# Kernel optimization log

Hardware: AMD Instinct MI355X
Metric: run time of the kernel (lower is better)

Reference implementation:

```python
import jax, jax.numpy as jnp
import numpy as np

N_NODES = 100_000
N_EDGES = 1_600_000
D_IN = 128
D_OUT = 128


def setup_inputs() -> dict:
    key = jax.random.key(0)
    ks = jax.random.split(key, 6)
    X = jax.random.normal(ks[0], (N_NODES, D_IN), dtype=jnp.float32)
    ref_a = jax.random.randint(ks[1], (N_EDGES,), 0, N_NODES, dtype=jnp.int64 if jax.config.jax_enable_x64 else jnp.int32)
    backref = jax.random.randint(ks[2], (N_EDGES,), 0, N_NODES, dtype=jnp.int64 if jax.config.jax_enable_x64 else jnp.int32)
    e_map = jax.random.randint(ks[3], (N_EDGES,), 0, N_NODES, dtype=jnp.int32)
    v_count = jnp.ones((1,), dtype=jnp.int32)
    # GlorotUniform init for the two projection matrices
    limit = np.sqrt(6.0 / (D_IN + D_OUT)).astype(np.float32)
    W = jax.random.uniform(ks[4], (D_IN, D_OUT), dtype=jnp.float32, minval=-limit, maxval=limit)
    W_prop = jax.random.uniform(ks[5], (D_IN, D_OUT), dtype=jnp.float32, minval=-limit, maxval=limit)
    b = jnp.zeros((D_OUT,), dtype=jnp.float32)
    return {"X": X, "ref_a": ref_a, "backref": backref, "e_map": e_map,
            "v_count": v_count, "W": W, "W_prop": W_prop, "b": b}


def reference(X, ref_a, backref, e_map, v_count, W, W_prop, b):
    # Dual linear projections
    XW = X @ W                 # [N, D_OUT]
    XW_prop = X @ W_prop       # [N, D_OUT]
    # wl1_convolution_compact: gather rows at edge sources, scatter-sum into targets
    msgs = XW_prop[ref_a]      # [E, D_OUT] irregular gather
    X_conv = jax.ops.segment_sum(msgs, backref, num_segments=X.shape[0])  # [N, D_OUT]
    # bias add + activation
    X_out = jax.nn.relu(XW + X_conv + b)
    return (X_out, ref_a, backref, e_map, v_count)
```

## Files before the change

kernel.cpp:

```cpp
#include <hip/hip_runtime.h>
#include <hip/hip_bf16.h>


#define SCAN_BE 1024

typedef __attribute__((ext_vector_type(8))) short bf16x8;
typedef __attribute__((ext_vector_type(4))) float f32x4;

__device__ __forceinline__ float bf2f(unsigned short u) {
    return __uint_as_float(((unsigned int)u) << 16);
}

__device__ __forceinline__ unsigned short f2bf(float f) {
    unsigned int b = __float_as_uint(f);
    unsigned int r = (b + 0x7FFFu + ((b >> 16) & 1u)) >> 16;
    return (unsigned short)r;
}

__device__ __forceinline__ unsigned char f2e4m3(float f) {
    unsigned int u = __float_as_uint(f);
    unsigned char s = (unsigned char)((u >> 24) & 0x80u);
    unsigned int ua = u & 0x7FFFFFFFu;
    float a = __uint_as_float(ua);
    if (!(a < 448.0f)) return (unsigned char)(s | 0x7E);
    if (a < 0x1p-10f) return s;
    int E = (int)(ua >> 23);
    int e = E - 120;
    unsigned int M = ua & 0x7FFFFFu;
    if (e >= 1) {
        unsigned int r = M + 0x7FFFFu + ((M >> 20) & 1u);
        unsigned int m = r >> 20;
        if (m >= 8) { m = 0; e++; }
        if (e >= 16 || (e == 15 && m == 7))
            return (unsigned char)(s | 0x7E);
        return (unsigned char)(s | (e << 3) | (m & 7));
    } else {
        int m = (int)(a * 512.0f + 0.5f);
        if (m >= 8) return (unsigned char)(s | 0x08);
        return (unsigned char)(s | m);
    }
}

__device__ __forceinline__ float4 load4f(const void* p, size_t off, int isbf) {
    if (isbf) {
        ushort4 u = *(const ushort4*)((const unsigned short*)p + off);
        return make_float4(bf2f(u.x), bf2f(u.y), bf2f(u.z), bf2f(u.w));
    }
    return *(const float4*)((const float*)p + off);
}

__global__ void detect_kernel(const unsigned int* __restrict__ Xw,
                              const unsigned int* __restrict__ bw,
                              int* __restrict__ flags) {
    __shared__ int c_bf16, c_i64;
    int t = threadIdx.x;
    if (t == 0) { c_bf16 = 0; c_i64 = 0; }
    __syncthreads();
    int local = 0;
    #pragma unroll
    for (int k = 0; k < 4; k++) {
        unsigned int w = Xw[t * 4 + k];
        unsigned int e = (w >> 7) & 0xFFu;
        if (e >= 96u && e <= 143u) local++;
    }
    atomicAdd(&c_bf16, local);
    atomicAdd(&c_i64, (bw[2 * t + 1] == 0u) ? 1 : 0);
    __syncthreads();
    if (t == 0) {
        flags[0] = (c_bf16 >= 512) ? 1 : 0;
        flags[1] = (c_i64 == 256) ? 1 : 0;
    }
}

__global__ void zero_kernel(float4* __restrict__ p, long long n4) {
    long long i = (long long)blockIdx.x * blockDim.x + threadIdx.x;
    long long stride = (long long)gridDim.x * blockDim.x;
    for (; i < n4; i += stride)
        p[i] = make_float4(0.f, 0.f, 0.f, 0.f);
}

__global__ void zero_i32(int* __restrict__ p, long long n) {
    long long i = (long long)blockIdx.x * blockDim.x + threadIdx.x;
    long long stride = (long long)gridDim.x * blockDim.x;
    for (; i < n; i += stride) p[i] = 0;
}

__global__ void fill_zero_f32(float* __restrict__ p, long long lo, long long hi) {
    long long i = lo + (long long)blockIdx.x * blockDim.x + threadIdx.x;
    long long stride = (long long)gridDim.x * blockDim.x;
    for (; i < hi; i += stride) p[i] = 0.f;
}

__global__ void xconv_kernel(const void* __restrict__ Xraw,
                             const int* __restrict__ flags,
                             unsigned short* __restrict__ Xb, long long n4) {
    long long i = (long long)blockIdx.x * blockDim.x + threadIdx.x;
    long long stride = (long long)gridDim.x * blockDim.x;
    const int isbf = flags[0];
    for (; i < n4; i += stride) {
        if (isbf) {
            *(ushort4*)(Xb + i * 4) = *((const ushort4*)Xraw + i);
        } else {
            float4 v = *((const float4*)Xraw + i);
            ushort4 u;
            u.x = f2bf(v.x); u.y = f2bf(v.y);
            u.z = f2bf(v.z); u.w = f2bf(v.w);
            *(ushort4*)(Xb + i * 4) = u;
        }
    }
}

__global__ void xconv_fp8_kernel(const void* __restrict__ Xraw,
                                 const int* __restrict__ flags,
                                 unsigned char* __restrict__ Xq, long long n4) {
    long long i = (long long)blockIdx.x * blockDim.x + threadIdx.x;
    long long stride = (long long)gridDim.x * blockDim.x;
    const int isbf = flags[0];
    for (; i < n4; i += stride) {
        float4 v = load4f(Xraw, (size_t)i * 4, isbf);
        uchar4 q;
        q.x = f2e4m3(v.x); q.y = f2e4m3(v.y);
        q.z = f2e4m3(v.z); q.w = f2e4m3(v.w);
        *(uchar4*)(Xq + i * 4) = q;
    }
}

__global__ void wtrans_frag_kernel(const void* __restrict__ W,
                                   const void* __restrict__ Wp,
                                   const void* __restrict__ bias,
                                   const int* __restrict__ flags,
                                   unsigned short* __restrict__ Wtf,
                                   unsigned short* __restrict__ Wptf,
                                   float* __restrict__ biasf, int D) {
    const int isbf = flags[0];
    int i = blockIdx.x * blockDim.x + threadIdx.x;
    if (i < 2048) {
        int lane = i & 63;
        int ctkc = i >> 6;
        int kc = ctkc & 3;
        int ct = ctkc >> 2;
        int lr = lane & 15, lg = lane >> 4;
        int n = ct * 16 + lr;
        #pragma unroll
        for (int e = 0; e < 8; e++) {
            int k = kc * 32 + 16 * (e >> 2) + 4 * lg + (e & 3);
            size_t src = (size_t)k * D + n;
            float w  = isbf ? bf2f(((const unsigned short*)W)[src])
                            : ((const float*)W)[src];
            float wp = isbf ? bf2f(((const unsigned short*)Wp)[src])
                            : ((const float*)Wp)[src];
            Wtf [(size_t)i * 8 + e] = f2bf(w);
            Wptf[(size_t)i * 8 + e] = f2bf(wp);
        }
    }
    if (i < D) {
        biasf[i] = isbf ? bf2f(((const unsigned short*)bias)[i])
                        : ((const float*)bias)[i];
    }
}

__global__ void copy_idx_kernel(const int* __restrict__ ref_a,
                                const int* __restrict__ backref,
                                const int* __restrict__ e_map,
                                const int* __restrict__ v_count,
                                const int* __restrict__ flags,
                                float* __restrict__ out,
                                long long base, long long E) {
    long long i = (long long)blockIdx.x * blockDim.x + threadIdx.x;
    const int is64 = flags[1];
    if (i < E) {
        out[base + i] = (float)ref_a[is64 ? 2 * i : i];
    } else if (i < 2 * E) {
        long long k = i - E;
        out[base + i] = (float)backref[is64 ? 2 * k : k];
    } else if (i < 3 * E) {
        out[base + i] = (float)e_map[i - 2 * E];
    } else if (i == 3 * E) {
        out[base + i] = (float)v_count[0];
    }
}

__global__ void hist_kernel(const int* __restrict__ dst,
                            const int* __restrict__ flags,
                            int* __restrict__ counts, long long E) {
    long long i = (long long)blockIdx.x * blockDim.x + threadIdx.x;
    long long stride = (long long)gridDim.x * blockDim.x;
    const int is64 = flags[1];
    for (; i < E; i += stride)
        atomicAdd(&counts[dst[is64 ? 2 * i : i]], 1);
}

__global__ __launch_bounds__(256) void block_reduce_kernel(
    const int* __restrict__ counts, int* __restrict__ bsum, int n) {
    __shared__ int sd[256];
    int b = blockIdx.x, t = threadIdx.x;
    int lo = b * SCAN_BE;
    int hi = lo + SCAN_BE; if (hi > n) hi = n;
    int s = 0;
    for (int i = lo + t; i < hi; i += 256) s += counts[i];
    sd[t] = s;
    __syncthreads();
    for (int d = 128; d > 0; d >>= 1) {
        if (t < d) sd[t] += sd[t + d];
        __syncthreads();
    }
    if (t == 0) bsum[b] = sd[0];
}

__global__ __launch_bounds__(1024) void scan_bsum_kernel(
    int* __restrict__ bsum, int nb, int* __restrict__ offsets, int n) {
    __shared__ int sd[1024];
    int t = threadIdx.x;
    int v = (t < nb) ? bsum[t] : 0;
    sd[t] = v;
    __syncthreads();
    for (int d = 1; d < 1024; d <<= 1) {
        int x = (t >= d) ? sd[t - d] : 0;
        __syncthreads();
        sd[t] += x;
        __syncthreads();
    }
    if (t < nb) bsum[t] = (t == 0) ? 0 : sd[t - 1];
    if (t == 1023) offsets[n] = sd[1023];
}

__global__ __launch_bounds__(256) void block_scan_kernel(
    const int* counts, const int* __restrict__ bsum,
    int* __restrict__ offsets, int* cursor, int n) {
    __shared__ int ts[256];
    int b = blockIdx.x, t = threadIdx.x;
    int base0 = b * SCAN_BE + t * 4;
    int c0 = (base0 + 0 < n) ? counts[base0 + 0] : 0;
    int c1 = (base0 + 1 < n) ? counts[base0 + 1] : 0;
    int c2 = (base0 + 2 < n) ? counts[base0 + 2] : 0;
    int c3 = (base0 + 3 < n) ? counts[base0 + 3] : 0;
    ts[t] = c0 + c1 + c2 + c3;
    __syncthreads();
    for (int d = 1; d < 256; d <<= 1) {
        int x = (t >= d) ? ts[t - d] : 0;
        __syncthreads();
        ts[t] += x;
        __syncthreads();
    }
    int ex = bsum[b] + (t ? ts[t - 1] : 0);
    if (base0 + 0 < n) { offsets[base0 + 0] = ex; cursor[base0 + 0] = ex; } ex += c0;
    if (base0 + 1 < n) { offsets[base0 + 1] = ex; cursor[base0 + 1] = ex; } ex += c1;
    if (base0 + 2 < n) { offsets[base0 + 2] = ex; cursor[base0 + 2] = ex; } ex += c2;
    if (base0 + 3 < n) { offsets[base0 + 3] = ex; cursor[base0 + 3] = ex; }
}

__global__ __launch_bounds__(1024) void scan_kernel(
    const int* counts, int* __restrict__ offsets, int* cursor, int n) {
    __shared__ int part[1024];
    int t = threadIdx.x;
    int chunk = (n + 1023) / 1024;
    int lo = t * chunk;
    int hi = lo + chunk; if (hi > n) hi = n;
    int s = 0;
    for (int i = lo; i < hi; i++) s += counts[i];
    part[t] = s;
    __syncthreads();
    for (int d = 1; d < 1024; d <<= 1) {
        int v = (t >= d) ? part[t - d] : 0;
        __syncthreads();
        part[t] += v;
        __syncthreads();
    }
    int run = (t == 0) ? 0 : part[t - 1];
    for (int i = lo; i < hi; i++) {
        int c = counts[i];
        offsets[i] = run;
        cursor[i]  = run;
        run += c;
    }
    if (t == 1023) offsets[n] = part[1023];
}

__global__ void scatter_xcd_kernel(const int* __restrict__ src,
                                   const int* __restrict__ dst,
                                   const int* __restrict__ flags,
                                   int* __restrict__ cursor,
                                   int* __restrict__ srcs,
                                   long long E, int N, int nstripes) {
    int b = blockIdx.x;
    int r = b & 7;
    int s = b >> 3;
    int rchunk = (N + 7) / 8;
    int rlo = r * rchunk;
    int rhi = rlo + rchunk; if (rhi > N) rhi = N;
    long long e0 = (long long)s * E / nstripes;
    long long e1 = (long long)(s + 1) * E / nstripes;
    const int is64 = flags[1];
    for (long long i = e0 + threadIdx.x; i < e1; i += blockDim.x) {
        long long ei = is64 ? 2 * i : i;
        int d = dst[ei];
        if (d < rlo || d >= rhi) continue;
        int sv = src[ei];
        int pos = atomicAdd(&cursor[d], 1);
        srcs[pos] = sv;
    }
}

__device__ __forceinline__ void acc_fp8x4(float4& acc, unsigned int q) {
    unsigned int b0 = ((q << 24) & 0x80000000u) | ((q << 20) & 0x07F00000u);
    unsigned int b1 = ((q << 16) & 0x80000000u) | ((q << 12) & 0x07F00000u);
    unsigned int b2 = ((q <<  8) & 0x80000000u) | ((q <<  4) & 0x07F00000u);
    unsigned int b3 = ( q        & 0x80000000u) | ((q >>  4) & 0x07F00000u);
    acc.x = fmaf(__uint_as_float(b0), 0x1p120f, acc.x);
    acc.y = fmaf(__uint_as_float(b1), 0x1p120f, acc.y);
    acc.z = fmaf(__uint_as_float(b2), 0x1p120f, acc.z);
    acc.w = fmaf(__uint_as_float(b3), 0x1p120f, acc.w);
}

__global__ void csr_agg_f8b_kernel(const unsigned char* __restrict__ Xq,
                                   const int* __restrict__ offsets,
                                   const int* __restrict__ srcs,
                                   unsigned short* __restrict__ Ab,
                                   int N, int D) {
    int g = (int)(((long long)blockIdx.x * blockDim.x + threadIdx.x) >> 5);
    int lane = threadIdx.x & 31;
    if (g >= N) return;
    int lo = offsets[g], hi = offsets[g + 1];
    for (int c = lane * 4; c < D; c += 128) {
        float4 acc = make_float4(0.f, 0.f, 0.f, 0.f);
        int i = lo;
        for (; i + 1 < hi; i += 2) {
            int s0 = srcs[i], s1 = srcs[i + 1];
            unsigned int q0 = *(const unsigned int*)(Xq + (size_t)s0 * D + c);
            unsigned int q1 = *(const unsigned int*)(Xq + (size_t)s1 * D + c);
            acc_fp8x4(acc, q0);
            acc_fp8x4(acc, q1);
        }
        if (i < hi) {
            int s0 = srcs[i];
            unsigned int q0 = *(const unsigned int*)(Xq + (size_t)s0 * D + c);
            acc_fp8x4(acc, q0);
        }
        ushort4 o;
        o.x = f2bf(acc.x); o.y = f2bf(acc.y);
        o.z = f2bf(acc.z); o.w = f2bf(acc.w);
        *(ushort4*)(Ab + (size_t)g * D + c) = o;
    }
}

__global__ void csr_agg_b2b_kernel(const unsigned short* __restrict__ Xb,
                                   const int* __restrict__ offsets,
                                   const int* __restrict__ srcs,
                                   unsigned short* __restrict__ Ab,
                                   int N, int D) {
    int g = (int)(((long long)blockIdx.x * blockDim.x + threadIdx.x) >> 5);
    int lane = threadIdx.x & 31;
    if (g >= N) return;
    int lo = offsets[g], hi = offsets[g + 1];
    for (int c = lane * 4; c < D; c += 128) {
        float4 acc = make_float4(0.f, 0.f, 0.f, 0.f);
        for (int i = lo; i < hi; i++) {
            int s = srcs[i];
            ushort4 u = *(const ushort4*)(Xb + (size_t)s * D + c);
            acc.x += bf2f(u.x); acc.y += bf2f(u.y);
            acc.z += bf2f(u.z); acc.w += bf2f(u.w);
        }
        ushort4 o;
        o.x = f2bf(acc.x); o.y = f2bf(acc.y);
        o.z = f2bf(acc.z); o.w = f2bf(acc.w);
        *(ushort4*)(Ab + (size_t)g * D + c) = o;
    }
}

__global__ void csr_agg_kernel(const void* __restrict__ Xraw,
                               const int* __restrict__ offsets,
                               const int* __restrict__ srcs,
                               const int* __restrict__ flags,
                               float* __restrict__ A, int N, int D) {
    int g = (int)(((long long)blockIdx.x * blockDim.x + threadIdx.x) >> 5);
    int lane = threadIdx.x & 31;
    if (g >= N) return;
    const int isbf = flags[0];
    int lo = offsets[g], hi = offsets[g + 1];
    for (int c = lane * 4; c < D; c += 128) {
        float4 acc = make_float4(0.f, 0.f, 0.f, 0.f);
        for (int i = lo; i < hi; i++) {
            int s = srcs[i];
            float4 v = load4f(Xraw, (size_t)s * D + c, isbf);
            acc.x += v.x; acc.y += v.y; acc.z += v.z; acc.w += v.w;
        }
        *(float4*)(A + (size_t)g * D + c) = acc;
    }
}

__global__ __launch_bounds__(256) void gemm_mfma_kernel(
    const unsigned short* __restrict__ Xb,
    const unsigned short* __restrict__ Ab,
    const unsigned short* __restrict__ Wtf,
    const unsigned short* __restrict__ Wptf,
    const float* __restrict__ biasf,
    float* __restrict__ out, long long Nw) {
    const int D = 128;
    const int wave = threadIdx.x >> 6;
    const int lane = threadIdx.x & 63;
    const int lr = lane & 15;
    const int lg = lane >> 4;
    const long long rbase = ((long long)blockIdx.x * 4 + wave) * 16;
    if (rbase >= Nw) return;

    long long arow = rbase + lr;
    if (arow >= Nw) arow = Nw - 1;
    const unsigned short* xrow = Xb + arow * D;
    const unsigned short* prow = Ab + arow * D;

    f32x4 acc[8];
    #pragma unroll
    for (int i = 0; i < 8; i++) acc[i] = (f32x4){0.f, 0.f, 0.f, 0.f};

    for (int kc = 0; kc < 8; kc++) {
        const bool xpart = (kc < 4);
        const unsigned short* arow_p = xpart ? xrow : prow;
        const unsigned short* wf     = xpart ? Wtf : Wptf;
        const int kk = kc & 3;
        const int k0 = kk * 32 + 4 * lg;

        ushort4 alo = *(const ushort4*)(arow_p + k0);
        ushort4 ahi = *(const ushort4*)(arow_p + k0 + 16);
        bf16x8 a = {(short)alo.x, (short)alo.y, (short)alo.z, (short)alo.w,
                    (short)ahi.x, (short)ahi.y, (short)ahi.z, (short)ahi.w};

        #pragma unroll
        for (int ct = 0; ct < 8; ct++) {
            bf16x8 b = *(const bf16x8*)(wf +
                           ((size_t)((ct * 4 + kk) * 64 + lane)) * 8);
            acc[ct] = __builtin_amdgcn_mfma_f32_16x16x32_bf16(a, b, acc[ct],
                                                              0, 0, 0);
        }
    }

    #pragma unroll
    for (int ct = 0; ct < 8; ct++) {
        int n = ct * 16 + lr;
        float bn = biasf[n];
        #pragma unroll
        for (int r = 0; r < 4; r++) {
            long long m = rbase + 4 * lg + r;
            if (m < Nw) {
                float v = acc[ct][r] + bn;
                out[m * D + n] = v > 0.f ? v : 0.f;
            }
        }
    }
}

__global__ void edge_agg_kernel(const void* __restrict__ Xraw,
                                const int* __restrict__ src,
                                const int* __restrict__ dst,
                                const int* __restrict__ flags,
                                float* __restrict__ A,
                                long long E, int D, int row0, int row1) {
    long long tid = (long long)blockIdx.x * blockDim.x + threadIdx.x;
    long long e = tid >> 5;
    int lane = (int)(tid & 31);
    if (e >= E) return;
    const int is64 = flags[1];
    const int isbf = flags[0];
    long long ei = is64 ? 2 * e : e;
    int d = dst[ei];
    if (d < row0 || d >= row1) return;
    int s = src[ei];
    for (int c = lane * 4; c < D; c += 128) {
        float4 v = load4f(Xraw, (size_t)s * D + c, isbf);
        float* a = A + (size_t)(d - row0) * D + c;
        atomicAdd(a + 0, v.x);
        atomicAdd(a + 1, v.y);
        atomicAdd(a + 2, v.z);
        atomicAdd(a + 3, v.w);
    }
}

__global__ __launch_bounds__(256) void gemm_fused_kernel(
    const void* __restrict__ Xraw, const float* __restrict__ A,
    const void* __restrict__ Wraw, const void* __restrict__ Wpraw,
    const void* __restrict__ braw, const int* __restrict__ flags,
    float* __restrict__ out, long long row0, long long rend) {
    const int D = 128;
    __shared__ float sX[64][68];
    __shared__ float sW[64][68];

    const long long rbase = row0 + (long long)blockIdx.x * 64;
    const int cbase = blockIdx.y * 64;
    const int t  = threadIdx.x;
    const int tx = t & 15;
    const int ty = t >> 4;
    const int isbf = flags[0];

    float acc[4][4] = {};

    for (int kk = 0; kk < 256; kk += 64) {
        const bool first = (kk < 128);
        const void* Ws = first ? Wraw : Wpraw;
        const int kc = kk & 127;

        #pragma unroll
        for (int i = 0; i < 4; i++) {
            int r  = ty + i * 16;
            int c4 = tx * 4;
            long long grow = rbase + r;
            float4 v = make_float4(0.f, 0.f, 0.f, 0.f);
            if (grow < rend) {
                if (first)
                    v = load4f(Xraw, (size_t)grow * D + kc + c4, isbf);
                else
                    v = *(const float4*)(A + (size_t)(grow - row0) * D + kc + c4);
            }
            *(float4*)&sX[r][c4] = v;
            float4 w = load4f(Ws, (size_t)(kc + r) * D + cbase + c4, isbf);
            *(float4*)&sW[r][c4] = w;
        }
        __syncthreads();

        #pragma unroll
        for (int k4 = 0; k4 < 16; k4++) {
            float4 xv[4], wv[4];
            #pragma unroll
            for (int i = 0; i < 4; i++)
                xv[i] = *(float4*)&sX[ty * 4 + i][k4 * 4];
            #pragma unroll
            for (int i = 0; i < 4; i++)
                wv[i] = *(float4*)&sW[k4 * 4 + i][tx * 4];
            #pragma unroll
            for (int ki = 0; ki < 4; ki++) {
                #pragma unroll
                for (int r = 0; r < 4; r++) {
                    float x = (ki == 0) ? xv[r].x
                            : (ki == 1) ? xv[r].y
                            : (ki == 2) ? xv[r].z
                                        : xv[r].w;
                    acc[r][0] += x * wv[ki].x;
                    acc[r][1] += x * wv[ki].y;
                    acc[r][2] += x * wv[ki].z;
                    acc[r][3] += x * wv[ki].w;
                }
            }
        }
        __syncthreads();
    }

    const long long grow0 = rbase + ty * 4;
    const int gcol0 = cbase + tx * 4;
    float b0, b1, b2, b3;
    if (isbf) {
        const unsigned short* bb = (const unsigned short*)braw;
        b0 = bf2f(bb[gcol0 + 0]); b1 = bf2f(bb[gcol0 + 1]);
        b2 = bf2f(bb[gcol0 + 2]); b3 = bf2f(bb[gcol0 + 3]);
    } else {
        const float* bb = (const float*)braw;
        b0 = bb[gcol0 + 0]; b1 = bb[gcol0 + 1];
        b2 = bb[gcol0 + 2]; b3 = bb[gcol0 + 3];
    }
    #pragma unroll
    for (int r = 0; r < 4; r++) {
        long long grow = grow0 + r;
        if (grow >= rend) break;
        float4 v;
        v.x = acc[r][0] + b0; v.x = v.x > 0.f ? v.x : 0.f;
        v.y = acc[r][1] + b1; v.y = v.y > 0.f ? v.y : 0.f;
        v.z = acc[r][2] + b2; v.z = v.z > 0.f ? v.z : 0.f;
        v.w = acc[r][3] + b3; v.w = v.w > 0.f ? v.w : 0.f;
        *(float4*)(out + (size_t)grow * D + gcol0) = v;
    }
}

extern "C" void kernel_launch(void* const* d_in, const int* in_sizes, int n_in,
                              void* d_out, int out_size, void* d_ws, size_t ws_size,
                              hipStream_t stream) {
    const void* X       = d_in[0];
    const int*  ref_a   = (const int*)d_in[1];
    const int*  backref = (const int*)d_in[2];
    const int*  e_map   = (const int*)d_in[3];
    const int*  v_count = (const int*)d_in[4];
    const void* W       = d_in[5];
    const void* W_prop  = d_in[6];
    const void* bias    = d_in[7];
    float* out = (float*)d_out;

    int Dout = (n_in > 7 && in_sizes[7] > 0) ? in_sizes[7] : 128;
    int Din  = (in_sizes[5] > 0 && in_sizes[5] % Dout == 0)
                   ? in_sizes[5] / Dout : Dout;
    long long N = in_sizes[0] / Din;
    long long E = in_sizes[1];
    long long base = (long long)out_size - 3 * E - 1;
    if (base < 0) base = N * Dout;

    auto align256 = [](size_t x) { return (x + 255) & ~(size_t)255; };
    size_t o_flags = 0;
    size_t o_off   = align256(o_flags + 256);
    size_t o_cur   = align256(o_off + (size_t)(N + 1) * 4);
    size_t o_bsum  = align256(o_cur + (size_t)N * 4);
    size_t o_srcs  = align256(o_bsum + 1024 * 4);
    size_t o_A     = align256(o_srcs + (size_t)E * 4);
    size_t o_Xb    = align256(o_A + (size_t)N * Din * 4);
    size_t o_Wt    = align256(o_Xb + (size_t)N * Din * 2);
    size_t o_Wpt   = align256(o_Wt + (size_t)Din * Dout * 2);
    size_t o_bf    = align256(o_Wpt + (size_t)Din * Dout * 2);
    size_t o_Xq    = align256(o_bf + (size_t)Dout * 4);
    size_t need_csr  = o_Xb;
    size_t need_mfma = o_Xq;
    size_t need_fp8  = o_Xq + (size_t)N * Din;
    const bool use_csr  = (ws_size >= need_csr);
    const bool use_mfma = (ws_size >= need_mfma) && (Din == 128) && (Dout == 128);
    const bool use_fp8  = (ws_size >= need_fp8) && use_mfma;

    char* wsb = (char*)d_ws;
    int*            flags   = (int*)(wsb + o_flags);
    int*            offsets = (int*)(wsb + o_off);
    int*            cursor  = (int*)(wsb + o_cur);
    int*            bsum    = (int*)(wsb + o_bsum);
    int*            srcs    = (int*)(wsb + o_srcs);
    float*          A       = use_csr ? (float*)(wsb + o_A) : (float*)(wsb + 256);
    unsigned short* Ab      = (unsigned short*)(wsb + o_A);
    unsigned short* Xb      = (unsigned short*)(wsb + o_Xb);
    unsigned short* Wtf     = (unsigned short*)(wsb + o_Wt);
    unsigned short* Wptf    = (unsigned short*)(wsb + o_Wpt);
    float*          biasf   = (float*)(wsb + o_bf);
    unsigned char*  Xq      = (unsigned char*)(wsb + o_Xq);

    detect_kernel<<<1, 256, 0, stream>>>((const unsigned int*)X,
                                         (const unsigned int*)backref, flags);

    {   long long total = 3 * E + 1;
        int blocks = (int)((total + 255) / 256);
        copy_idx_kernel<<<blocks, 256, 0, stream>>>(ref_a, backref, e_map,
                                                    v_count, flags, out,
                                                    base, E);
    }

    long long Nw = N;
    long long cap = base / Dout;
    if (cap < Nw) Nw = cap;
    if (N * Dout < base)
        fill_zero_f32<<<2048, 1024, 0, stream>>>(out, N * Dout, base);

    if (use_csr) {
        zero_i32<<<256, 256, 0, stream>>>(cursor, N);
        hist_kernel<<<2048, 256, 0, stream>>>(backref, flags, cursor, E);
        int nb = (int)((N + SCAN_BE - 1) / SCAN_BE);
        if (nb <= 1024) {
            block_reduce_kernel<<<nb, 256, 0, stream>>>(cursor, bsum, (int)N);
            scan_bsum_kernel<<<1, 1024, 0, stream>>>(bsum, nb, offsets, (int)N);
            block_scan_kernel<<<nb, 256, 0, stream>>>(cursor, bsum, offsets,
                                                      cursor, (int)N);
        } else {
            scan_kernel<<<1, 1024, 0, stream>>>(cursor, offsets, cursor, (int)N);
        }
        {
            const int nstripes = 256;
            scatter_xcd_kernel<<<8 * nstripes, 256, 0, stream>>>(
                ref_a, backref, flags, cursor, srcs, E, (int)N, nstripes);
        }

        if (use_mfma) {
            {
                long long n4 = (N * (long long)Din) / 4;
                int cblocks = (int)((n4 + 1023) / 1024);
                if (cblocks > 2048) cblocks = 2048;
                xconv_kernel<<<cblocks, 1024, 0, stream>>>(X, flags, Xb, n4);
                if (use_fp8)
                    xconv_fp8_kernel<<<cblocks, 1024, 0, stream>>>(X, flags,
                                                                   Xq, n4);
            }
            wtrans_frag_kernel<<<8, 256, 0, stream>>>(W, W_prop, bias, flags,
                                                      Wtf, Wptf, biasf, Din);
            {
                long long threads = N * 32;
                int blocks = (int)((threads + 255) / 256);
                if (use_fp8)
                    csr_agg_f8b_kernel<<<blocks, 256, 0, stream>>>(
                        Xq, offsets, srcs, Ab, (int)N, Din);
                else
                    csr_agg_b2b_kernel<<<blocks, 256, 0, stream>>>(
                        Xb, offsets, srcs, Ab, (int)N, Din);
            }
            {
                int blocks = (int)((Nw + 63) / 64);
                gemm_mfma_kernel<<<blocks, 256, 0, stream>>>(Xb, Ab, Wtf, Wptf,
                                                             biasf, out, Nw);
            }
        } else {
            {
                long long threads = N * 32;
                int blocks = (int)((threads + 255) / 256);
                csr_agg_kernel<<<blocks, 256, 0, stream>>>(X, offsets, srcs,
                                                           flags, A, (int)N, Din);
            }
            dim3 grid((unsigned)((Nw + 63) / 64), 2);
            gemm_fused_kernel<<<grid, 256, 0, stream>>>(X, A, W, W_prop, bias,
                                                        flags, out, 0, Nw);
        }
    } else {
        size_t avail = (ws_size > 256) ? ws_size - 256 : 0;
        size_t rows_cap = avail / ((size_t)Din * sizeof(float));
        long long rows_per;
        if (rows_cap >= (size_t)Nw) rows_per = Nw > 0 ? Nw : 1;
        else {
            rows_per = (long long)(rows_cap & ~(size_t)63);
            if (rows_per <= 0) rows_per = 64;
        }
        for (long long row0 = 0; row0 < Nw; row0 += rows_per) {
            long long rows = (Nw - row0 < rows_per) ? (Nw - row0) : rows_per;
            long long rend = row0 + rows;
            {   long long n4 = (rows * (long long)Din) / 4;
                int blocks = (int)((n4 + 1023) / 1024);
                if (blocks > 2048) blocks = 2048;
                if (blocks > 0)
                    zero_kernel<<<blocks, 1024, 0, stream>>>((float4*)A, n4);
            }
            {   long long threads = E * 32;
                int blocks = (int)((threads + 255) / 256);
                edge_agg_kernel<<<blocks, 256, 0, stream>>>(X, ref_a, backref,
                                                            flags, A, E, Din,
                                                            (int)row0, (int)rend);
            }
            {   dim3 grid((unsigned)((rows + 63) / 64), 2);
                gemm_fused_kernel<<<grid, 256, 0, stream>>>(X, A, W, W_prop,
                                                            bias, flags, out,
                                                            row0, rend);
            }
        }
    }
}
```

Measured before the change: 297.8 us.

## Replace XCD-striped CSR scatter with two-pass bucket sort, fuse histogram and conversions

Builds the CSR source list with a two-pass bucketed scatter. Edges are first appended as packed (dst,src) pairs into 64-node buckets, then each bucket is scattered locally into per-node slots, replacing the XCD-striped scatter. The edge histogram is folded into the index-copy kernel, and the bf16 and fp8 conversions of X are merged into one pass that reads X once. This adds an 8-byte-per-edge pairs buffer and an extra pass over the edges, in exchange for more local atomics and writes.

```diff
diff --git a/kernel.cpp b/kernel.cpp
--- a/kernel.cpp
+++ b/kernel.cpp
@@ -3,6 +3,7 @@
 
 
 #define SCAN_BE 1024
+#define BSH 6
 
 typedef __attribute__((ext_vector_type(8))) short bf16x8;
 typedef __attribute__((ext_vector_type(4))) float f32x4;
@@ -91,37 +92,26 @@
     for (; i < hi; i += stride) p[i] = 0.f;
 }
 
-__global__ void xconv_kernel(const void* __restrict__ Xraw,
-                             const int* __restrict__ flags,
-                             unsigned short* __restrict__ Xb, long long n4) {
-    long long i = (long long)blockIdx.x * blockDim.x + threadIdx.x;
-    long long stride = (long long)gridDim.x * blockDim.x;
-    const int isbf = flags[0];
-    for (; i < n4; i += stride) {
-        if (isbf) {
-            *(ushort4*)(Xb + i * 4) = *((const ushort4*)Xraw + i);
-        } else {
-            float4 v = *((const float4*)Xraw + i);
-            ushort4 u;
-            u.x = f2bf(v.x); u.y = f2bf(v.y);
-            u.z = f2bf(v.z); u.w = f2bf(v.w);
-            *(ushort4*)(Xb + i * 4) = u;
-        }
-    }
-}
-
-__global__ void xconv_fp8_kernel(const void* __restrict__ Xraw,
-                                 const int* __restrict__ flags,
-                                 unsigned char* __restrict__ Xq, long long n4) {
+__global__ void xconv_dual_kernel(const void* __restrict__ Xraw,
+                                  const int* __restrict__ flags,
+                                  unsigned short* __restrict__ Xb,
+                                  unsigned char* __restrict__ Xq,
+                                  int writeq, long long n4) {
     long long i = (long long)blockIdx.x * blockDim.x + threadIdx.x;
     long long stride = (long long)gridDim.x * blockDim.x;
     const int isbf = flags[0];
     for (; i < n4; i += stride) {
         float4 v = load4f(Xraw, (size_t)i * 4, isbf);
-        uchar4 q;
-        q.x = f2e4m3(v.x); q.y = f2e4m3(v.y);
-        q.z = f2e4m3(v.z); q.w = f2e4m3(v.w);
-        *(uchar4*)(Xq + i * 4) = q;
+        ushort4 u;
+        u.x = f2bf(v.x); u.y = f2bf(v.y);
+        u.z = f2bf(v.z); u.w = f2bf(v.w);
+        *(ushort4*)(Xb + i * 4) = u;
+        if (writeq) {
+            uchar4 q;
+            q.x = f2e4m3(v.x); q.y = f2e4m3(v.y);
+            q.z = f2e4m3(v.z); q.w = f2e4m3(v.w);
+            *(uchar4*)(Xq + i * 4) = q;
+        }
     }
 }
 
@@ -159,17 +149,19 @@
     }
 }
 
-__global__ void copy_idx_kernel(const int* __restrict__ ref_a,
-                                const int* __restrict__ backref,
-                                const int* __restrict__ e_map,
-                                const int* __restrict__ v_count,
-                                const int* __restrict__ flags,
-                                float* __restrict__ out,
-                                long long base, long long E) {
+__global__ void copy_idx_hist_kernel(const int* __restrict__ ref_a,
+                                     const int* __restrict__ backref,
+                                     const int* __restrict__ e_map,
+                                     const int* __restrict__ v_count,
+                                     const int* __restrict__ flags,
+                                     float* __restrict__ out,
+                                     int* __restrict__ counts,
+                                     long long base, long long E) {
     long long i = (long long)blockIdx.x * blockDim.x + threadIdx.x;
     const int is64 = flags[1];
     if (i < E) {
         out[base + i] = (float)ref_a[is64 ? 2 * i : i];
+        atomicAdd(&counts[backref[is64 ? 2 * i : i]], 1);
     } else if (i < 2 * E) {
         long long k = i - E;
         out[base + i] = (float)backref[is64 ? 2 * k : k];
@@ -178,16 +170,6 @@
     } else if (i == 3 * E) {
         out[base + i] = (float)v_count[0];
     }
-}
-
-__global__ void hist_kernel(const int* __restrict__ dst,
-                            const int* __restrict__ flags,
-                            int* __restrict__ counts, long long E) {
-    long long i = (long long)blockIdx.x * blockDim.x + threadIdx.x;
-    long long stride = (long long)gridDim.x * blockDim.x;
-    const int is64 = flags[1];
-    for (; i < E; i += stride)
-        atomicAdd(&counts[dst[is64 ? 2 * i : i]], 1);
 }
 
 __global__ __launch_bounds__(256) void block_reduce_kernel(
@@ -274,6 +256,51 @@
         run += c;
     }
     if (t == 1023) offsets[n] = part[1023];
+}
+
+__global__ void binit_kernel(const int* __restrict__ offsets,
+                             int* __restrict__ bcur, int nbk, int N) {
+    int b = blockIdx.x * blockDim.x + threadIdx.x;
+    if (b < nbk) {
+        int node = b << BSH;
+        if (node > N) node = N;
+        bcur[b] = offsets[node];
+    }
+}
+
+__global__ void bucket_pass1_kernel(const int* __restrict__ src,
+                                    const int* __restrict__ dst,
+                                    const int* __restrict__ flags,
+                                    int* __restrict__ bcur,
+                                    long long* __restrict__ pairs,
+                                    long long E) {
+    long long i = (long long)blockIdx.x * blockDim.x + threadIdx.x;
+    long long stride = (long long)gridDim.x * blockDim.x;
+    const int is64 = flags[1];
+    for (; i < E; i += stride) {
+        long long ei = is64 ? 2 * i : i;
+        int d = dst[ei];
+        int s = src[ei];
+        int pos = atomicAdd(&bcur[d >> BSH], 1);
+        pairs[pos] = ((long long)d << 32) | (unsigned int)s;
+    }
+}
+
+__global__ __launch_bounds__(256) void bucket_pass2_kernel(
+    const long long* __restrict__ pairs, const int* __restrict__ offsets,
+    int* __restrict__ cursor, int* __restrict__ srcs, int N) {
+    int b = blockIdx.x;
+    int n0 = b << BSH;
+    int n1 = n0 + (1 << BSH); if (n1 > N) n1 = N;
+    if (n0 >= N) return;
+    int lo = offsets[n0], hi = offsets[n1];
+    for (int i = lo + threadIdx.x; i < hi; i += blockDim.x) {
+        long long p = pairs[i];
+        int d = (int)(p >> 32);
+        int s = (int)(p & 0xFFFFFFFFll);
+        int pos = atomicAdd(&cursor[d], 1);
+        srcs[pos] = s;
+    }
 }
 
 __global__ void scatter_xcd_kernel(const int* __restrict__ src,
@@ -474,6 +501,27 @@
     }
 }
 
+__global__ void copy_idx_kernel(const int* __restrict__ ref_a,
+                                const int* __restrict__ backref,
+                                const int* __restrict__ e_map,
+                                const int* __restrict__ v_count,
+                                const int* __restrict__ flags,
+                                float* __restrict__ out,
+                                long long base, long long E) {
+    long long i = (long long)blockIdx.x * blockDim.x + threadIdx.x;
+    const int is64 = flags[1];
+    if (i < E) {
+        out[base + i] = (float)ref_a[is64 ? 2 * i : i];
+    } else if (i < 2 * E) {
+        long long k = i - E;
+        out[base + i] = (float)backref[is64 ? 2 * k : k];
+    } else if (i < 3 * E) {
+        out[base + i] = (float)e_map[i - 2 * E];
+    } else if (i == 3 * E) {
+        out[base + i] = (float)v_count[0];
+    }
+}
+
 __global__ __launch_bounds__(256) void gemm_fused_kernel(
     const void* __restrict__ Xraw, const float* __restrict__ A,
     const void* __restrict__ Wraw, const void* __restrict__ Wpraw,
@@ -587,6 +635,7 @@
     long long E = in_sizes[1];
     long long base = (long long)out_size - 3 * E - 1;
     if (base < 0) base = N * Dout;
+    int nbk = (int)((N + (1 << BSH) - 1) >> BSH);
 
     auto align256 = [](size_t x) { return (x + 255) & ~(size_t)255; };
     size_t o_flags = 0;
@@ -600,12 +649,16 @@
     size_t o_Wpt   = align256(o_Wt + (size_t)Din * Dout * 2);
     size_t o_bf    = align256(o_Wpt + (size_t)Din * Dout * 2);
     size_t o_Xq    = align256(o_bf + (size_t)Dout * 4);
+    size_t o_bcur  = align256(o_Xq + (size_t)N * Din);
+    size_t o_pairs = align256(o_bcur + (size_t)(nbk + 1) * 4);
     size_t need_csr  = o_Xb;
     size_t need_mfma = o_Xq;
-    size_t need_fp8  = o_Xq + (size_t)N * Din;
+    size_t need_fp8  = o_bcur;
+    size_t need_bkt  = o_pairs + (size_t)E * 8;
     const bool use_csr  = (ws_size >= need_csr);
     const bool use_mfma = (ws_size >= need_mfma) && (Din == 128) && (Dout == 128);
     const bool use_fp8  = (ws_size >= need_fp8) && use_mfma;
+    const bool use_bkt  = (ws_size >= need_bkt) && use_csr;
 
     char* wsb = (char*)d_ws;
     int*            flags   = (int*)(wsb + o_flags);
@@ -620,16 +673,11 @@
     unsigned short* Wptf    = (unsigned short*)(wsb + o_Wpt);
     float*          biasf   = (float*)(wsb + o_bf);
     unsigned char*  Xq      = (unsigned char*)(wsb + o_Xq);
+    int*            bcur    = (int*)(wsb + o_bcur);
+    long long*      pairs   = (long long*)(wsb + o_pairs);
 
     detect_kernel<<<1, 256, 0, stream>>>((const unsigned int*)X,
                                          (const unsigned int*)backref, flags);
-
-    {   long long total = 3 * E + 1;
-        int blocks = (int)((total + 255) / 256);
-        copy_idx_kernel<<<blocks, 256, 0, stream>>>(ref_a, backref, e_map,
-                                                    v_count, flags, out,
-                                                    base, E);
-    }
 
     long long Nw = N;
     long long cap = base / Dout;
@@ -639,7 +687,12 @@
 
     if (use_csr) {
         zero_i32<<<256, 256, 0, stream>>>(cursor, N);
-        hist_kernel<<<2048, 256, 0, stream>>>(backref, flags, cursor, E);
+        {
+            long long total = 3 * E + 1;
+            int blocks = (int)((total + 255) / 256);
+            copy_idx_hist_kernel<<<blocks, 256, 0, stream>>>(
+                ref_a, backref, e_map, v_count, flags, out, cursor, base, E);
+        }
         int nb = (int)((N + SCAN_BE - 1) / SCAN_BE);
         if (nb <= 1024) {
             block_reduce_kernel<<<nb, 256, 0, stream>>>(cursor, bsum, (int)N);
@@ -649,7 +702,14 @@
         } else {
             scan_kernel<<<1, 1024, 0, stream>>>(cursor, offsets, cursor, (int)N);
         }
-        {
+        if (use_bkt) {
+            binit_kernel<<<(nbk + 255) / 256, 256, 0, stream>>>(offsets, bcur,
+                                                                nbk, (int)N);
+            bucket_pass1_kernel<<<2048, 256, 0, stream>>>(ref_a, backref, flags,
+                                                          bcur, pairs, E);
+            bucket_pass2_kernel<<<nbk, 256, 0, stream>>>(pairs, offsets,
+                                                         cursor, srcs, (int)N);
+        } else {
             const int nstripes = 256;
             scatter_xcd_kernel<<<8 * nstripes, 256, 0, stream>>>(
                 ref_a, backref, flags, cursor, srcs, E, (int)N, nstripes);
@@ -660,10 +720,8 @@
                 long long n4 = (N * (long long)Din) / 4;
                 int cblocks = (int)((n4 + 1023) / 1024);
                 if (cblocks > 2048) cblocks = 2048;
-                xconv_kernel<<<cblocks, 1024, 0, stream>>>(X, flags, Xb, n4);
-                if (use_fp8)
-                    xconv_fp8_kernel<<<cblocks, 1024, 0, stream>>>(X, flags,
-                                                                   Xq, n4);
+                xconv_dual_kernel<<<cblocks, 1024, 0, stream>>>(
+                    X, flags, Xb, Xq, use_fp8 ? 1 : 0, n4);
             }
             wtrans_frag_kernel<<<8, 256, 0, stream>>>(W, W_prop, bias, flags,
                                                       Wtf, Wptf, biasf, Din);
@@ -694,6 +752,13 @@
                                                         flags, out, 0, Nw);
         }
     } else {
+        {
+            long long total = 3 * E + 1;
+            int blocks = (int)((total + 255) / 256);
+            copy_idx_kernel<<<blocks, 256, 0, stream>>>(ref_a, backref, e_map,
+                                                        v_count, flags, out,
+                                                        base, E);
+        }
         size_t avail = (ws_size > 256) ? ws_size - 256 : 0;
         size_t rows_cap = avail / ((size_t)Din * sizeof(float));
         long long rows_per;
```

Result: slower. 496.8 us (+66.8%).
